# Optimization experiments

Measured on AMD Instinct MI355X. Metric: run time of the kernel, lower is better.

Reference implementation:

```python
import jax, jax.numpy as jnp
import numpy as np

B, N, DM = 4, 4096, 768
H, LH = 12, 4          # total heads, local heads
GH = H - LH            # global (FAVOR+) heads
DH = DM // H           # 64, head dim
M = 256                # nb random features
W = 128                # local window size
EPS = 1e-4


def _gaussian_orthogonal_matrix(m, d, rng):
    # performer-pytorch gaussian_orthogonal_random_matrix, scaling=0
    blocks = []
    for _ in range(int(np.ceil(m / d))):
        q, _ = np.linalg.qr(rng.standard_normal((d, d)))
        blocks.append(q.T)
    mat = np.concatenate(blocks, 0)[:m]
    multiplier = np.linalg.norm(rng.standard_normal((m, d)), axis=-1)
    return (multiplier[:, None] * mat).astype(np.float32)


def setup_inputs() -> dict:
    key = jax.random.key(0)
    ks = jax.random.split(key, 6)
    s = 0.02
    x = jax.random.normal(ks[0], (B, N, DM), jnp.float32)
    mask = jnp.ones((B, N), dtype=bool)
    Wq = jax.random.normal(ks[1], (DM, DM), jnp.float32) * s
    Wk = jax.random.normal(ks[2], (DM, DM), jnp.float32) * s
    Wv = jax.random.normal(ks[3], (DM, DM), jnp.float32) * s
    Wo = jax.random.normal(ks[4], (DM, DM), jnp.float32) * s
    bo = jnp.zeros((DM,), jnp.float32)
    proj = jnp.asarray(_gaussian_orthogonal_matrix(M, DH, np.random.default_rng(0)))
    return {"x": x, "mask": mask, "Wq": Wq, "Wk": Wk, "Wv": Wv,
            "Wo": Wo, "bo": bo, "proj": proj}


def _softmax_kernel(data, proj, is_query):
    # FAVOR+ positive random features for the softmax kernel
    d = data.shape[-1]
    normalizer = d ** -0.25
    ratio = proj.shape[0] ** -0.5
    dd = jnp.einsum('bhnd,md->bhnm', data * normalizer, proj)
    diag = jnp.sum(data ** 2, axis=-1) * 0.5 * (normalizer ** 2)  # (b,h,n)
    if is_query:
        stab = jnp.max(dd, axis=-1, keepdims=True)
        return ratio * (jnp.exp(dd - diag[..., None] - stab) + EPS)
    stab = jnp.max(dd)
    return ratio * (jnp.exp(dd - diag[..., None] - stab) + EPS)


def _favor_attention(q, k, v, proj):
    # non-causal linear attention: O(n * m * d)
    qp = _softmax_kernel(q, proj, True)    # (b,gh,n,m)
    kp = _softmax_kernel(k, proj, False)   # (b,gh,n,m)
    k_sum = kp.sum(axis=2)                               # (b,gh,m)
    d_inv = 1.0 / jnp.einsum('bhnm,bhm->bhn', qp, k_sum)
    context = jnp.einsum('bhnm,bhnd->bhmd', kp, v)       # (b,gh,m,d)
    return jnp.einsum('bhmd,bhnm,bhn->bhnd', context, qp, d_inv)


def _rotary(x):
    # SinusoidalEmbeddings + apply_rotary_pos_emb (NeoX half-rotation)
    n, d = x.shape[-2], x.shape[-1]
    half = d // 2
    inv_freq = 1.0 / (10000.0 ** (jnp.arange(0, d, 2, dtype=jnp.float32) / d))
    freqs = jnp.arange(n, dtype=jnp.float32)[:, None] * inv_freq[None, :]
    emb = jnp.concatenate([freqs, freqs], axis=-1)       # (n,d)
    cos, sin = jnp.cos(emb), jnp.sin(emb)
    x1, x2 = x[..., :half], x[..., half:]
    rot = jnp.concatenate([-x2, x1], axis=-1)
    return x * cos + rot * sin


def _local_attention(lq, lk, lv, mask):
    # windowed attention, look_backward=1, look_forward=1 (non-causal)
    b, h, n, d = lq.shape
    lq, lk = _rotary(lq), _rotary(lk)
    nw = n // W
    bq = lq.reshape(b, h, nw, W, d)
    bk = lk.reshape(b, h, nw, W, d)
    bv = lv.reshape(b, h, nw, W, d)

    def look5(t):  # gather previous/current/next window along window axis
        p = jnp.pad(t, ((0, 0), (0, 0), (1, 1), (0, 0), (0, 0)))
        return jnp.concatenate([p[:, :, i:i + nw] for i in range(3)], axis=3)

    bk, bv = look5(bk), look5(bv)                        # (b,h,nw,3W,d)
    dots = jnp.einsum('bhwie,bhwje->bhwij', bq, bk) * (d ** -0.5)

    ticker = jnp.arange(n).reshape(nw, W)
    tp = jnp.pad(ticker, ((1, 1), (0, 0)), constant_values=-1)
    bq_k = jnp.concatenate([tp[i:i + nw] for i in range(3)], axis=1)  # (nw,3W)
    pad_ok = (bq_k != -1)[None, None, :, None, :]

    mq = mask.reshape(b, nw, W)
    mkp = jnp.pad(mq, ((0, 0), (1, 1), (0, 0)), constant_values=False)
    mk = jnp.concatenate([mkp[:, i:i + nw] for i in range(3)], axis=2)  # (b,nw,3W)
    inp_ok = (mq[:, :, :, None] & mk[:, :, None, :])[:, None]          # (b,1,nw,W,3W)

    neg = -jnp.finfo(dots.dtype).max
    dots = jnp.where(pad_ok & inp_ok, dots, neg)
    attn = jax.nn.softmax(dots, axis=-1)
    out = jnp.einsum('bhwij,bhwje->bhwie', attn, bv)
    return out.reshape(b, h, n, d)


def reference(x, mask, Wq, Wk, Wv, Wo, bo, proj):
    b, n, _ = x.shape
    split = lambda t: t.reshape(b, n, H, DH).transpose(0, 2, 1, 3)  # (b,h,n,d)
    q, k, v = split(x @ Wq), split(x @ Wk), split(x @ Wv)
    qg, lq = q[:, :GH], q[:, GH:]
    kg, lk = k[:, :GH], k[:, GH:]
    vg, lv = v[:, :GH], v[:, GH:]
    # global heads: zero masked values, FAVOR+ linear attention
    vg = jnp.where(mask[:, None, :, None], vg, 0.0)
    out_g = _favor_attention(qg, kg, vg, proj)
    out_l = _local_attention(lq, lk, lv, mask)
    out = jnp.concatenate([out_g, out_l], axis=1)        # (b,H,n,d)
    out = out.transpose(0, 2, 1, 3).reshape(b, n, DM)
    return out @ Wo + bo
```

## Files before the change

### kernel.cpp

```cpp
#include <hip/hip_runtime.h>
#include <hip/hip_fp16.h>
#include <math.h>

#define BB 4
#define NN 4096
#define DMM 768
#define HHH 12
#define LHH 4
#define GHH 8
#define DH 64
#define MM 256
#define WW 128
#define NWIN (NN/WW)
#define EPSF 1.0e-4f
#define NRM 0.35355339059327373f
#define NRM2 0.125f
#define RATIO 0.0625f
#define LN1E4_32 0.28782313662425572f
#define KSTAB_BLOCKS (BB * GHH * (NN / 64))

using fp16x8 = __attribute__((ext_vector_type(8))) _Float16;
using f32x4  = __attribute__((ext_vector_type(4))) float;

static __device__ __forceinline__ unsigned short f2h(float x) {
  return __half_as_ushort(__float2half(x));
}
static __device__ __forceinline__ void gload16(const unsigned short* g, unsigned short* l) {
  __builtin_amdgcn_global_load_lds(
      (const __attribute__((address_space(1))) void*)g,
      (__attribute__((address_space(3))) void*)l, 16, 0, 0);
}

__global__ __launch_bounds__(256) void w_split(
    const float* __restrict__ W, unsigned short* __restrict__ Whi)
{
  int o = blockIdx.x * 256 + threadIdx.x;
  int k = o / DMM, n = o % DMM;
  Whi[(size_t)n * DMM + k] = f2h(W[o]);
}

__global__ __launch_bounds__(256) void a_split(
    const float* __restrict__ A, unsigned short* __restrict__ Ahi,
    unsigned short* __restrict__ Alo)
{
  size_t o = ((size_t)blockIdx.x * 256 + threadIdx.x) * 4;
  float4 v = *(const float4*)(A + o);
  float f[4] = {v.x, v.y, v.z, v.w};
  unsigned short hi[4], lo[4];
#pragma unroll
  for (int i = 0; i < 4; ++i) {
    __half h = __float2half(f[i]);
    hi[i] = __half_as_ushort(h);
    lo[i] = f2h(f[i] - __half2float(h));
  }
  *(uint2*)(Ahi + o) = *(uint2*)&hi[0];
  *(uint2*)(Alo + o) = *(uint2*)&lo[0];
}

__global__ __launch_bounds__(256) void gemm_mfma(
    const float* __restrict__ A, const unsigned short* __restrict__ Bhi,
    const float* __restrict__ bias, float* __restrict__ C, int K, int Nc)
{
  __shared__ unsigned short Ah[128][40];
  __shared__ unsigned short Al[128][40];
  __shared__ unsigned short Bh[128][40];

  const int tid = threadIdx.x;
  const int wid = tid >> 6, lane = tid & 63;
  const int quad = lane >> 4, l16 = lane & 15;
  const int row0 = blockIdx.y * 128;
  const int col0 = blockIdx.x * 128;
  const int wm = (wid & 1) * 64, wn = (wid >> 1) * 64;
  const int sr = tid >> 1;
  const int sk = (tid & 1) * 16;

  f32x4 acc[4][4];
  const f32x4 zf = {0.f, 0.f, 0.f, 0.f};
#pragma unroll
  for (int i = 0; i < 4; ++i)
#pragma unroll
    for (int j = 0; j < 4; ++j) acc[i][j] = zf;

  for (int k0 = 0; k0 < K; k0 += 32) {
    __syncthreads();
    {
      const float* a = A + (size_t)(row0 + sr) * K + k0 + sk;
      float fv[16];
      *(float4*)&fv[0]  = *(const float4*)(a);
      *(float4*)&fv[4]  = *(const float4*)(a + 4);
      *(float4*)&fv[8]  = *(const float4*)(a + 8);
      *(float4*)&fv[12] = *(const float4*)(a + 12);
      unsigned hw[8], lw[8];
#pragma unroll
      for (int p = 0; p < 8; ++p) {
        float x0 = fv[2 * p], x1 = fv[2 * p + 1];
        __half h0 = __float2half(x0), h1 = __float2half(x1);
        unsigned short l0 = f2h(x0 - __half2float(h0));
        unsigned short l1 = f2h(x1 - __half2float(h1));
        hw[p] = (unsigned)__half_as_ushort(h0) | ((unsigned)__half_as_ushort(h1) << 16);
        lw[p] = (unsigned)l0 | ((unsigned)l1 << 16);
      }
      *(uint4*)&Ah[sr][sk]     = *(uint4*)&hw[0];
      *(uint4*)&Ah[sr][sk + 8] = *(uint4*)&hw[4];
      *(uint4*)&Al[sr][sk]     = *(uint4*)&lw[0];
      *(uint4*)&Al[sr][sk + 8] = *(uint4*)&lw[4];
    }
    {
      const unsigned short* bh = Bhi + (size_t)(col0 + sr) * DMM + k0 + sk;
      *(uint4*)&Bh[sr][sk]     = *(const uint4*)(bh);
      *(uint4*)&Bh[sr][sk + 8] = *(const uint4*)(bh + 8);
    }
    __syncthreads();

    fp16x8 afh[4], afl[4], bfh[4];
#pragma unroll
    for (int t = 0; t < 4; ++t) {
      afh[t] = *(const fp16x8*)&Ah[wm + t * 16 + l16][quad * 8];
      afl[t] = *(const fp16x8*)&Al[wm + t * 16 + l16][quad * 8];
      bfh[t] = *(const fp16x8*)&Bh[wn + t * 16 + l16][quad * 8];
    }
#pragma unroll
    for (int ti = 0; ti < 4; ++ti)
#pragma unroll
      for (int tj = 0; tj < 4; ++tj) {
        acc[ti][tj] = __builtin_amdgcn_mfma_f32_16x16x32_f16(afh[ti], bfh[tj], acc[ti][tj], 0, 0, 0);
        acc[ti][tj] = __builtin_amdgcn_mfma_f32_16x16x32_f16(afl[ti], bfh[tj], acc[ti][tj], 0, 0, 0);
      }
  }

  float bv[4] = {0.f, 0.f, 0.f, 0.f};
  if (bias) {
#pragma unroll
    for (int tj = 0; tj < 4; ++tj) bv[tj] = bias[col0 + wn + tj * 16 + l16];
  }
#pragma unroll
  for (int ti = 0; ti < 4; ++ti) {
    const int gr = row0 + wm + ti * 16 + quad * 4;
#pragma unroll
    for (int tj = 0; tj < 4; ++tj) {
      const int gc = col0 + wn + tj * 16 + l16;
      float* cp = C + (size_t)gr * Nc + gc;
#pragma unroll
      for (int r = 0; r < 4; ++r)
        cp[(size_t)r * Nc] = acc[ti][tj][r] + bv[tj];
    }
  }
}

__global__ __launch_bounds__(256) void gemm_mfma_pre(
    const unsigned short* __restrict__ Ahi, const unsigned short* __restrict__ Alo,
    const unsigned short* __restrict__ Bhi,
    const float* __restrict__ bias, float* __restrict__ C, int K, int Nc)
{
  __shared__ unsigned short Ah[128][32];
  __shared__ unsigned short Al[128][32];
  __shared__ unsigned short Bh[128][32];

  const int tid = threadIdx.x;
  const int wid = tid >> 6, lane = tid & 63;
  const int quad = lane >> 4, l16 = lane & 15;

  const int nwg = gridDim.x * gridDim.y;
  int hw = blockIdx.y * gridDim.x + blockIdx.x;
  int logical = ((nwg & 7) == 0) ? ((hw & 7) * (nwg >> 3) + (hw >> 3)) : hw;
  const int col0 = (logical % gridDim.x) * 128;
  const int row0 = (logical / gridDim.x) * 128;

  const int wm = (wid & 1) * 64, wn = (wid >> 1) * 64;
  const int sw8 = (quad ^ ((l16 >> 1) & 3)) * 8;
// ... 42 lines not shown
        acc[ti][tj] = __builtin_amdgcn_mfma_f32_16x16x32_f16(afl[ti], bfh[tj], acc[ti][tj], 0, 0, 0);
      }
  }

  float bv[4] = {0.f, 0.f, 0.f, 0.f};
  if (bias) {
#pragma unroll
    for (int tj = 0; tj < 4; ++tj) bv[tj] = bias[col0 + wn + tj * 16 + l16];
  }
#pragma unroll
  for (int ti = 0; ti < 4; ++ti) {
    const int gr = row0 + wm + ti * 16 + quad * 4;
#pragma unroll
    for (int tj = 0; tj < 4; ++tj) {
      const int gc = col0 + wn + tj * 16 + l16;
      float* cp = C + (size_t)gr * Nc + gc;
#pragma unroll
      for (int r = 0; r < 4; ++r)
        cp[(size_t)r * Nc] = acc[ti][tj][r] + bv[tj];
    }
  }
}

__global__ __launch_bounds__(256) void transpose_proj(
    const float* __restrict__ proj,
    unsigned short* __restrict__ phh, unsigned short* __restrict__ phl)
{
  int o = blockIdx.x * 256 + threadIdx.x;
  int k = o >> 8, m = o & 255;
  float v = proj[m * 64 + k];
  __half hh = __float2half(v);
  float lf = v - __half2float(hh);
  phh[m * 64 + k] = __half_as_ushort(hh);
  phl[m * 64 + k] = f2h(lf);
}

__global__ __launch_bounds__(256) void rot_qk(
    const float* __restrict__ Qb, const float* __restrict__ Kb,
    unsigned short* __restrict__ Qlh, unsigned short* __restrict__ Klh)
{
  int idx = blockIdx.x * 256 + threadIdx.x;
  int n = idx & (NN - 1);
  int bh = idx >> 12;
  int b = bh >> 2, h = bh & 3;
  const float* qs = Qb + ((size_t)(b * NN + n)) * DMM + GHH * DH + h * DH;
  const float* ks = Kb + ((size_t)(b * NN + n)) * DMM + GHH * DH + h * DH;
  float q[64], k[64];
#pragma unroll
  for (int t = 0; t < 16; ++t) {
    *(float4*)&q[t * 4] = *(const float4*)(qs + t * 4);
    *(float4*)&k[t * 4] = *(const float4*)(ks + t * 4);
  }
  unsigned short qo[64], ko[64];
#pragma unroll
  for (int i = 0; i < 32; ++i) {
    float invf = __expf((float)i * -LN1E4_32);
    float th = (float)n * invf;
    float s, c;
    sincosf(th, &s, &c);
    qo[i]      = f2h(fmaf(q[i], c, -q[i + 32] * s) * NRM2);
    qo[i + 32] = f2h(fmaf(q[i + 32], c, q[i] * s) * NRM2);
    ko[i]      = f2h(fmaf(k[i], c, -k[i + 32] * s));
    ko[i + 32] = f2h(fmaf(k[i + 32], c, k[i] * s));
  }
  unsigned short* qd = Qlh + (size_t)idx * 64;
  unsigned short* kd = Klh + (size_t)idx * 64;
#pragma unroll
  for (int t = 0; t < 8; ++t) {
    *(uint4*)(qd + t * 8) = *(uint4*)&qo[t * 8];
    *(uint4*)(kd + t * 8) = *(uint4*)&ko[t * 8];
  }
}

__global__ __launch_bounds__(256) void v_trans(
    const float* __restrict__ Vb, unsigned short* __restrict__ Vt)
{
  __shared__ unsigned short T[64][72];
  const int nb = blockIdx.x, h = blockIdx.y, b = blockIdx.z;
  const int n0 = nb * 64;
  const int tid = threadIdx.x;
  {
    int r = tid >> 2, g = tid & 3;
    const float* src = Vb + ((size_t)(b * NN + n0 + r)) * DMM + GHH * DH + h * DH + g * 16;
#pragma unroll
    for (int t = 0; t < 4; ++t) {
      float4 v = *(const float4*)(src + t * 4);
      T[g * 16 + t * 4 + 0][r] = f2h(v.x);
      T[g * 16 + t * 4 + 1][r] = f2h(v.y);
      T[g * 16 + t * 4 + 2][r] = f2h(v.z);
      T[g * 16 + t * 4 + 3][r] = f2h(v.w);
    }
  }
  __syncthreads();
  {
    int d = tid >> 2, g = tid & 3;
    unsigned short* dst = Vt + ((size_t)(b * LHH + h) * DH + d) * NN + n0 + g * 16;
    *(uint4*)dst       = *(uint4*)&T[d][g * 16];
    *(uint4*)(dst + 8) = *(uint4*)&T[d][g * 16 + 8];
  }
}

__global__ __launch_bounds__(256) void local_attn2(
    const unsigned short* __restrict__ Qlh, const unsigned short* __restrict__ Klh,
    const unsigned short* __restrict__ Vt, float* __restrict__ Qb)
{
  __shared__ unsigned short Pl[4][32][72];
  const int w = blockIdx.x, h = blockIdx.y, b = blockIdx.z;
  const int tid = threadIdx.x;
  const int wid = tid >> 6, lane = tid & 63;
  const int quad = lane >> 4, l16 = lane & 15;
  const int bh = b * LHH + h;
  const int qn0 = w * WW + wid * 32;

  fp16x8 Aq[2][2];
#pragma unroll
  for (int mt = 0; mt < 2; ++mt)
#pragma unroll
    for (int ks = 0; ks < 2; ++ks)
      Aq[mt][ks] = *(const fp16x8*)(Qlh + ((size_t)bh * NN + qn0 + mt * 16 + l16) * 64 + ks * 32 + quad * 8);

  float m_run[8], l_run[8];
  f32x4 Oacc[2][4];
  const f32x4 zf = {0.f, 0.f, 0.f, 0.f};
#pragma unroll
  for (int r = 0; r < 8; ++r) { m_run[r] = -3.4e38f; l_run[r] = 0.f; }
#pragma unroll
  for (int mt = 0; mt < 2; ++mt)
// ... 68 lines not shown
        fp16x8 Ap[2];
#pragma unroll
        for (int mt = 0; mt < 2; ++mt)
          Ap[mt] = *(const fp16x8*)&Pl[wid][mt * 16 + l16][kstep * 32 + quad * 8];
        fp16x8 Bv[4];
#pragma unroll
        for (int nt = 0; nt < 4; ++nt)
          Bv[nt] = *(const fp16x8*)(Vt + ((size_t)bh * DH + nt * 16 + l16) * NN + kn0 + kstep * 32 + quad * 8);
#pragma unroll
        for (int mt = 0; mt < 2; ++mt)
#pragma unroll
          for (int nt = 0; nt < 4; ++nt)
            Oacc[mt][nt] = __builtin_amdgcn_mfma_f32_16x16x32_f16(Ap[mt], Bv[nt], Oacc[mt][nt], 0, 0, 0);
      }
    }
  }

#pragma unroll
  for (int mt = 0; mt < 2; ++mt)
#pragma unroll
    for (int reg = 0; reg < 4; ++reg) {
      const float inv = 1.0f / l_run[mt * 4 + reg];
      const int n = qn0 + mt * 16 + quad * 4 + reg;
      float* dst = Qb + ((size_t)(b * NN + n)) * DMM + GHH * DH + h * DH;
#pragma unroll
      for (int nt = 0; nt < 4; ++nt)
        dst[nt * 16 + l16] = Oacc[mt][nt][reg] * inv;
    }
}

__global__ __launch_bounds__(256) void favor_kstab_mfma(
    const float* __restrict__ Kg, const unsigned short* __restrict__ phh,
    const unsigned short* __restrict__ phl, float* __restrict__ stabp)
{
  __shared__ unsigned short Khh[64][72];
  __shared__ unsigned short Khl[64][72];
  __shared__ float wred[4];
  const int tid = threadIdx.x;
  const int wid = tid >> 6, lane = tid & 63;
  const int quad = lane >> 4, l16 = lane & 15;
  const int chunk = blockIdx.x & 63;
  const int bh = blockIdx.x >> 6;
  const int b = bh >> 3, h = bh & 7;
  const int n0 = chunk * 64;
  const f32x4 zf = {0.f, 0.f, 0.f, 0.f};

  {
    const int r = tid >> 2, s2 = tid & 3;
    const float* ksrc = Kg + ((size_t)(b * NN + n0 + r)) * DMM + h * DH + s2 * 16;
    unsigned short th[16], tl[16];
#pragma unroll
    for (int t = 0; t < 4; ++t) {
      float4 g = *(const float4*)(ksrc + t * 4);
      float f[4] = {g.x * NRM, g.y * NRM, g.z * NRM, g.w * NRM};
#pragma unroll
      for (int j = 0; j < 4; ++j) {
        __half hh = __float2half(f[j]);
        th[t * 4 + j] = __half_as_ushort(hh);
        tl[t * 4 + j] = f2h(f[j] - __half2float(hh));
      }
    }
    *(uint4*)&Khh[r][s2 * 16]     = *(uint4*)&th[0];
    *(uint4*)&Khh[r][s2 * 16 + 8] = *(uint4*)&th[8];
    *(uint4*)&Khl[r][s2 * 16]     = *(uint4*)&tl[0];
    *(uint4*)&Khl[r][s2 * 16 + 8] = *(uint4*)&tl[8];
  }
  __syncthreads();

  const int wn0 = wid * 64;
  f32x4 acc[4][4];
#pragma unroll
  for (int i = 0; i < 4; ++i)
#pragma unroll
    for (int j = 0; j < 4; ++j) acc[i][j] = zf;

#pragma unroll
  for (int ks = 0; ks < 2; ++ks) {
    fp16x8 afh[4], afl[4], bfh[4], bfl[4];
#pragma unroll
    for (int t = 0; t < 4; ++t) {
      afh[t] = *(const fp16x8*)&Khh[t * 16 + l16][ks * 32 + quad * 8];
      afl[t] = *(const fp16x8*)&Khl[t * 16 + l16][ks * 32 + quad * 8];
      const size_t po = (size_t)(wn0 + t * 16 + l16) * 64 + ks * 32 + quad * 8;
      bfh[t] = *(const fp16x8*)(phh + po);
      bfl[t] = *(const fp16x8*)(phl + po);
    }
#pragma unroll
    for (int mt = 0; mt < 4; ++mt)
// ... 16 lines not shown
  for (int off = 32; off; off >>= 1) mx = fmaxf(mx, __shfl_xor(mx, off));
  if (lane == 0) wred[wid] = mx;
  __syncthreads();
  if (tid == 0)
    stabp[blockIdx.x] = fmaxf(fmaxf(wred[0], wred[1]), fmaxf(wred[2], wred[3]));
}

__global__ __launch_bounds__(256) void stab_reduce(
    const float* __restrict__ stabp, float* __restrict__ stab_f)
{
  __shared__ float wred[4];
  const int tid = threadIdx.x;
  float m = -3.4e38f;
  for (int i = tid; i < KSTAB_BLOCKS; i += 256) m = fmaxf(m, stabp[i]);
#pragma unroll
  for (int off = 32; off; off >>= 1) m = fmaxf(m, __shfl_xor(m, off));
  if ((tid & 63) == 0) wred[tid >> 6] = m;
  __syncthreads();
  if (tid == 0)
    *stab_f = fmaxf(fmaxf(wred[0], wred[1]), fmaxf(wred[2], wred[3]));
}

__global__ __launch_bounds__(256, 2) void favor_ctx_mfma(
    const float* __restrict__ Kg, const float* __restrict__ Vg,
    const unsigned short* __restrict__ phh, const unsigned short* __restrict__ phl,
    const float* __restrict__ stab_f,
    float* __restrict__ ctxp, float* __restrict__ ksump, int split)
{
  __shared__ unsigned short Khh[64][72];
  __shared__ unsigned short Khl[64][72];
  __shared__ unsigned short Vt_h[64][72];
  __shared__ unsigned short kp_s[256][72];
  __shared__ float diag_s[64];

  const int tid = threadIdx.x;
  const int wid = tid >> 6, lane = tid & 63;
  const int quad = lane >> 4, l16 = lane & 15;
  const int sidx = blockIdx.x % split;
  const int bh = blockIdx.x / split;
  const int b = bh >> 3, h = bh & 7;
  const int rows = NN / split, nch = rows / 64;
  const float stab = *stab_f;
  const int wn0 = wid * 64;
  const f32x4 zf = {0.f, 0.f, 0.f, 0.f};

  f32x4 acc2[4][4];
#pragma unroll
  for (int i = 0; i < 4; ++i)
#pragma unroll
    for (int j = 0; j < 4; ++j) acc2[i][j] = zf;
  float ksacc[4] = {0.f, 0.f, 0.f, 0.f};

  for (int c = 0; c < nch; ++c) {
    const int n0 = sidx * rows + c * 64;
    __syncthreads();
    {
      const int r = tid >> 2, s2 = tid & 3;
      const float* ksrc = Kg + ((size_t)(b * NN + n0 + r)) * DMM + h * DH + s2 * 16;
      const float* vsrc = Vg + ((size_t)(b * NN + n0 + r)) * DMM + h * DH + s2 * 16;
      float kq = 0.f;
      unsigned short th[16], tl[16];
#pragma unroll
      for (int t = 0; t < 4; ++t) {
        float4 g = *(const float4*)(ksrc + t * 4);
        float f[4] = {g.x * NRM, g.y * NRM, g.z * NRM, g.w * NRM};
#pragma unroll
        for (int j = 0; j < 4; ++j) {
          kq = fmaf(f[j], f[j], kq);
          __half hh = __float2half(f[j]);
          th[t * 4 + j] = __half_as_ushort(hh);
          tl[t * 4 + j] = f2h(f[j] - __half2float(hh));
        }
        float4 vv = *(const float4*)(vsrc + t * 4);
        Vt_h[s2 * 16 + t * 4 + 0][r] = f2h(vv.x);
        Vt_h[s2 * 16 + t * 4 + 1][r] = f2h(vv.y);
        Vt_h[s2 * 16 + t * 4 + 2][r] = f2h(vv.z);
        Vt_h[s2 * 16 + t * 4 + 3][r] = f2h(vv.w);
      }
      *(uint4*)&Khh[r][s2 * 16]     = *(uint4*)&th[0];
      *(uint4*)&Khh[r][s2 * 16 + 8] = *(uint4*)&th[8];
      *(uint4*)&Khl[r][s2 * 16]     = *(uint4*)&tl[0];
      *(uint4*)&Khl[r][s2 * 16 + 8] = *(uint4*)&tl[8];
      kq += __shfl_xor(kq, 1);
      kq += __shfl_xor(kq, 2);
      if (s2 == 0) diag_s[r] = 0.5f * kq;
    }
    __syncthreads();

    f32x4 acc[4][4];
#pragma unroll
    for (int i = 0; i < 4; ++i)
#pragma unroll
      for (int j = 0; j < 4; ++j) acc[i][j] = zf;
#pragma unroll
    for (int ks = 0; ks < 2; ++ks) {
      fp16x8 afh[4], afl[4], bfh[4], bfl[4];
#pragma unroll
      for (int t = 0; t < 4; ++t) {
        afh[t] = *(const fp16x8*)&Khh[t * 16 + l16][ks * 32 + quad * 8];
        afl[t] = *(const fp16x8*)&Khl[t * 16 + l16][ks * 32 + quad * 8];
        const size_t po = (size_t)(wn0 + t * 16 + l16) * 64 + ks * 32 + quad * 8;
        bfh[t] = *(const fp16x8*)(phh + po);
        bfl[t] = *(const fp16x8*)(phl + po);
      }
#pragma unroll
      for (int mt = 0; mt < 4; ++mt)
#pragma unroll
        for (int nt = 0; nt < 4; ++nt) {
// ... 68 lines not shown
}

__global__ __launch_bounds__(256) void favor_reduce(
    const float* __restrict__ ctxp, const float* __restrict__ ksump,
    unsigned short* __restrict__ ctxT_h, float* __restrict__ ksum, int split)
{
  int i = blockIdx.x * 256 + threadIdx.x;
  if (i < BB * GHH * MM * DH) {
    int bh = i / (MM * DH);
    int md = i % (MM * DH);
    float s = 0.f;
    for (int k = 0; k < split; ++k) s += ctxp[((size_t)(bh * split + k)) * MM * DH + md];
    ctxT_h[i] = f2h(s);
  }
  if (i < BB * GHH * MM) {
    int bh = i / MM, m = i % MM;
    float s = 0.f;
    for (int k = 0; k < split; ++k) s += ksump[(bh * split + k) * MM + m];
    ksum[i] = s;
  }
}

__global__ __launch_bounds__(256, 4) void favor_out_mfma(
    float* __restrict__ Q, const unsigned short* __restrict__ phh,
    const unsigned short* __restrict__ phl,
    const unsigned short* __restrict__ ctxT_h, const float* __restrict__ ksum)
{
  __shared__ union {
    struct { unsigned short Qhh[64][72]; unsigned short Qhl[64][72]; } a;
    unsigned short qp[64][264];
  } sm;
  __shared__ float red[4][64];
  __shared__ float dred[4][64];
  __shared__ float diag4[64][4];
  __shared__ float diag_s[64];
  __shared__ float dinv_s[64];
  __shared__ float ksum_s[256];

  const int tid = threadIdx.x;
  const int wid = tid >> 6, lane = tid & 63;
  const int quad = lane >> 4, l16 = lane & 15;
  const int bh = blockIdx.x >> 6;
  const int chunk = blockIdx.x & 63;
  const int b = bh >> 3, h = bh & 7;
  const int n0 = chunk * 64;
  const f32x4 zf = {0.f, 0.f, 0.f, 0.f};

  {
    const int r = tid >> 2, s2 = tid & 3;
    const float* src = Q + ((size_t)(b * NN + n0 + r)) * DMM + h * DH + s2 * 16;
    float sq = 0.f;
    unsigned short th[16], tl[16];
#pragma unroll
    for (int t = 0; t < 4; ++t) {
      float4 g = *(const float4*)(src + t * 4);
      float f[4] = {g.x * NRM, g.y * NRM, g.z * NRM, g.w * NRM};
#pragma unroll
      for (int j = 0; j < 4; ++j) {
        sq = fmaf(f[j], f[j], sq);
        __half hh = __float2half(f[j]);
        th[t * 4 + j] = __half_as_ushort(hh);
        tl[t * 4 + j] = f2h(f[j] - __half2float(hh));
      }
    }
    diag4[r][s2] = sq;
    *(uint4*)&sm.a.Qhh[r][s2 * 16]     = *(uint4*)&th[0];
    *(uint4*)&sm.a.Qhh[r][s2 * 16 + 8] = *(uint4*)&th[8];
    *(uint4*)&sm.a.Qhl[r][s2 * 16]     = *(uint4*)&tl[0];
    *(uint4*)&sm.a.Qhl[r][s2 * 16 + 8] = *(uint4*)&tl[8];
    ksum_s[tid] = ksum[bh * MM + tid];
  }
  __syncthreads();
  if (tid < 64)
    diag_s[tid] = 0.5f * (diag4[tid][0] + diag4[tid][1] + diag4[tid][2] + diag4[tid][3]);

  const int wn0 = wid * 64;
  f32x4 acc[4][4];
#pragma unroll
  for (int i = 0; i < 4; ++i)
#pragma unroll
    for (int j = 0; j < 4; ++j) acc[i][j] = zf;

#pragma unroll
  for (int ks = 0; ks < 2; ++ks) {
    fp16x8 afh[4], afl[4], bfh[4], bfl[4];
#pragma unroll
    for (int t = 0; t < 4; ++t) {
      afh[t] = *(const fp16x8*)&sm.a.Qhh[t * 16 + l16][ks * 32 + quad * 8];
      afl[t] = *(const fp16x8*)&sm.a.Qhl[t * 16 + l16][ks * 32 + quad * 8];
      const size_t po = (size_t)(wn0 + t * 16 + l16) * 64 + ks * 32 + quad * 8;
      bfh[t] = *(const fp16x8*)(phh + po);
      bfl[t] = *(const fp16x8*)(phl + po);
    }
#pragma unroll
    for (int mt = 0; mt < 4; ++mt)
#pragma unroll
      for (int nt = 0; nt < 4; ++nt) {
// ... 50 lines not shown

  const int wn2 = wid * 16;
  f32x4 acc2[4];
#pragma unroll
  for (int mt = 0; mt < 4; ++mt) acc2[mt] = zf;
#pragma unroll
  for (int ksp = 0; ksp < 8; ++ksp) {
    fp16x8 bv = *(const fp16x8*)(ctxT_h + ((size_t)bh * DH + wn2 + l16) * MM + ksp * 32 + quad * 8);
    fp16x8 ap[4];
#pragma unroll
    for (int mt = 0; mt < 4; ++mt)
      ap[mt] = *(const fp16x8*)&sm.qp[mt * 16 + l16][ksp * 32 + quad * 8];
#pragma unroll
    for (int mt = 0; mt < 4; ++mt)
      acc2[mt] = __builtin_amdgcn_mfma_f32_16x16x32_f16(ap[mt], bv, acc2[mt], 0, 0, 0);
  }
  __syncthreads();

#pragma unroll
  for (int mt = 0; mt < 4; ++mt)
#pragma unroll
    for (int reg = 0; reg < 4; ++reg) {
      const int row = mt * 16 + quad * 4 + reg;
      Q[((size_t)(b * NN + n0 + row)) * DMM + h * DH + wn2 + l16] =
          acc2[mt][reg] * dinv_s[row];
    }
}

extern "C" void kernel_launch(void* const* d_in, const int* in_sizes, int n_in,
                              void* d_out, int out_size, void* d_ws, size_t ws_size,
                              hipStream_t stream)
{
  (void)in_sizes; (void)n_in; (void)out_size;
  const float* x    = (const float*)d_in[0];
  const float* Wq   = (const float*)d_in[2];
  const float* Wk   = (const float*)d_in[3];
  const float* Wv   = (const float*)d_in[4];
  const float* Wo   = (const float*)d_in[5];
  const float* bo   = (const float*)d_in[6];
  const float* proj = (const float*)d_in[7];
  float* out = (float*)d_out;

  const size_t WSZ = (size_t)DMM * DMM;
  const size_t XSP = (size_t)BB * NN * DMM;
  const size_t wbuf_f = (4 * WSZ * 2 + 3) / 4;
  const size_t LSZ = (size_t)BB * LHH * NN * DH;
  const size_t lbuf_f = (3 * LSZ * 2 + 3) / 4;
  const size_t fixed_f = (size_t)3 * XSP + (size_t)BB * GHH * MM * DH
                       + (size_t)BB * GHH * MM + KSTAB_BLOCKS + 16 + MM * DH + 16
                       + wbuf_f + 16 + lbuf_f + 16;

  int split = 8, use_pre = 0;
  for (int s = 32; s >= 8; s >>= 1) {
    size_t part = (size_t)BB * GHH * s * (MM * DH + MM);
    size_t region = part > XSP ? part : XSP;
    if ((fixed_f + region) * 4 <= ws_size) { split = s; use_pre = 1; break; }
  }
  if (!use_pre) {
    for (int s = 32; s >= 8; s >>= 1) {
      size_t need = (fixed_f + (size_t)BB * GHH * s * (MM * DH + MM)) * 4;
      if (need <= ws_size) { split = s; break; }
    }
  }
  size_t part_f = (size_t)BB * GHH * split * (MM * DH + MM);
  size_t region_f = (use_pre && XSP > part_f) ? XSP : part_f;

  float* Qb    = (float*)d_ws;
  float* Kb    = Qb + XSP;
  float* Vb    = Kb + XSP;
  float* region = Vb + XSP;
  float* ctxp  = region;
  float* ksump = ctxp + (size_t)BB * GHH * split * MM * DH;
  unsigned short* xH = (unsigned short*)region;
  unsigned short* xL = xH + XSP;
  float* ctx   = region + region_f;
  unsigned short* ctxT_h = (unsigned short*)ctx;
  float* ksum  = ctx + (size_t)BB * GHH * MM * DH;
  float* stabp = ksum + BB * GHH * MM;
  float* stab_f = stabp + KSTAB_BLOCKS;
  unsigned short* proj_hh = (unsigned short*)(stab_f + 16);
  unsigned short* proj_hl = proj_hh + MM * DH;
  unsigned short* wsp = proj_hl + MM * DH;
  unsigned short* WqH = wsp;
  unsigned short* WkH = wsp + WSZ;
  unsigned short* WvH = wsp + 2 * WSZ;
  unsigned short* WoH = wsp + 3 * WSZ;
  unsigned short* Qlh = wsp + 4 * WSZ;
  unsigned short* Klh = Qlh + LSZ;
  unsigned short* Vtl = Klh + LSZ;

  dim3 blk(256);
  dim3 mg(DMM / 128, (BB * NN) / 128);
  const int wgrid = (int)(WSZ / 256);
  const int agrid = (int)(XSP / 1024);

  w_split<<<wgrid, blk, 0, stream>>>(Wq, WqH);
  w_split<<<wgrid, blk, 0, stream>>>(Wk, WkH);
  w_split<<<wgrid, blk, 0, stream>>>(Wv, WvH);
  w_split<<<wgrid, blk, 0, stream>>>(Wo, WoH);
  if (use_pre) {
    a_split<<<agrid, blk, 0, stream>>>(x, xH, xL);
    gemm_mfma_pre<<<mg, blk, 0, stream>>>(xH, xL, WqH, nullptr, Qb, DMM, DMM);
    gemm_mfma_pre<<<mg, blk, 0, stream>>>(xH, xL, WkH, nullptr, Kb, DMM, DMM);
    gemm_mfma_pre<<<mg, blk, 0, stream>>>(xH, xL, WvH, nullptr, Vb, DMM, DMM);
  } else {
    gemm_mfma<<<mg, blk, 0, stream>>>(x, WqH, nullptr, Qb, DMM, DMM);
    gemm_mfma<<<mg, blk, 0, stream>>>(x, WkH, nullptr, Kb, DMM, DMM);
    gemm_mfma<<<mg, blk, 0, stream>>>(x, WvH, nullptr, Vb, DMM, DMM);
  }
  rot_qk<<<(BB * LHH * NN) / 256, blk, 0, stream>>>(Qb, Kb, Qlh, Klh);
  v_trans<<<dim3(NN / 64, LHH, BB), blk, 0, stream>>>(Vb, Vtl);
  transpose_proj<<<64, blk, 0, stream>>>(proj, proj_hh, proj_hl);
  favor_kstab_mfma<<<KSTAB_BLOCKS, blk, 0, stream>>>(Kb, proj_hh, proj_hl, stabp);
  stab_reduce<<<1, blk, 0, stream>>>(stabp, stab_f);
  favor_ctx_mfma<<<BB * GHH * split, blk, 0, stream>>>(Kb, Vb, proj_hh, proj_hl, stab_f, ctxp, ksump, split);
  favor_reduce<<<(BB * GHH * MM * DH) / 256, blk, 0, stream>>>(ctxp, ksump, ctxT_h, ksum, split);
  favor_out_mfma<<<BB * GHH * (NN / 64), blk, 0, stream>>>(Qb, proj_hh, proj_hl, ctxT_h, ksum);
  local_attn2<<<dim3(NWIN, LHH, BB), blk, 0, stream>>>(Qlh, Klh, Vtl, Qb);
  if (use_pre) {
    a_split<<<agrid, blk, 0, stream>>>(Qb, xH, xL);
    gemm_mfma_pre<<<mg, blk, 0, stream>>>(xH, xL, WoH, bo, out, DMM, DMM);
  } else {
    gemm_mfma<<<mg, blk, 0, stream>>>(Qb, WoH, bo, out, DMM, DMM);
  }
}
```

Before: 534.8 us.

## Store Q/K/V projections as fp16 hi/lo pairs and fuse attention-output splitting

The QKV GEMMs now write fp16 hi/lo split outputs directly, V as hi only, instead of fp32. All downstream kernels read these half-precision buffers, so the per-kernel fp32-to-fp16 split work and fp32 traffic go away. The NRM scaling is folded into the projection matrix, with the diag terms rescaled by NRM2 to match. The favor and local attention kernels write their outputs as split hi/lo directly, which removes the separate a_split pass before the output GEMM. The fallback non-pre GEMM path is deleted, and V rounded to a single fp16 slightly changes numerics in the global heads.

```diff
diff --git a/kernel.cpp b/kernel.cpp
--- a/kernel.cpp
+++ b/kernel.cpp
@@ -25,6 +25,10 @@
 static __device__ __forceinline__ unsigned short f2h(float x) {
   return __half_as_ushort(__float2half(x));
 }
+static __device__ __forceinline__ float h2f(unsigned short u) {
+  union { unsigned short s; _Float16 f; } cv; cv.s = u;
+  return (float)cv.f;
+}
 static __device__ __forceinline__ void gload16(const unsigned short* g, unsigned short* l) {
   __builtin_amdgcn_global_load_lds(
       (const __attribute__((address_space(1))) void*)g,
@@ -49,102 +53,11 @@
   unsigned short hi[4], lo[4];
 #pragma unroll
   for (int i = 0; i < 4; ++i) {
-    __half h = __float2half(f[i]);
-    hi[i] = __half_as_ushort(h);
-    lo[i] = f2h(f[i] - __half2float(h));
+    hi[i] = f2h(f[i]);
+    lo[i] = f2h(f[i] - h2f(hi[i]));
   }
   *(uint2*)(Ahi + o) = *(uint2*)&hi[0];
   *(uint2*)(Alo + o) = *(uint2*)&lo[0];
-}
-
-__global__ __launch_bounds__(256) void gemm_mfma(
-    const float* __restrict__ A, const unsigned short* __restrict__ Bhi,
-    const float* __restrict__ bias, float* __restrict__ C, int K, int Nc)
-{
-  __shared__ unsigned short Ah[128][40];
-  __shared__ unsigned short Al[128][40];
-  __shared__ unsigned short Bh[128][40];
-
-  const int tid = threadIdx.x;
-  const int wid = tid >> 6, lane = tid & 63;
-  const int quad = lane >> 4, l16 = lane & 15;
-  const int row0 = blockIdx.y * 128;
-  const int col0 = blockIdx.x * 128;
-  const int wm = (wid & 1) * 64, wn = (wid >> 1) * 64;
-  const int sr = tid >> 1;
-  const int sk = (tid & 1) * 16;
-
-  f32x4 acc[4][4];
-  const f32x4 zf = {0.f, 0.f, 0.f, 0.f};
-#pragma unroll
-  for (int i = 0; i < 4; ++i)
-#pragma unroll
-    for (int j = 0; j < 4; ++j) acc[i][j] = zf;
-
-  for (int k0 = 0; k0 < K; k0 += 32) {
-    __syncthreads();
-    {
-      const float* a = A + (size_t)(row0 + sr) * K + k0 + sk;
-      float fv[16];
-      *(float4*)&fv[0]  = *(const float4*)(a);
-      *(float4*)&fv[4]  = *(const float4*)(a + 4);
-      *(float4*)&fv[8]  = *(const float4*)(a + 8);
-      *(float4*)&fv[12] = *(const float4*)(a + 12);
-      unsigned hw[8], lw[8];
-#pragma unroll
-      for (int p = 0; p < 8; ++p) {
-        float x0 = fv[2 * p], x1 = fv[2 * p + 1];
-        __half h0 = __float2half(x0), h1 = __float2half(x1);
-        unsigned short l0 = f2h(x0 - __half2float(h0));
-        unsigned short l1 = f2h(x1 - __half2float(h1));
-        hw[p] = (unsigned)__half_as_ushort(h0) | ((unsigned)__half_as_ushort(h1) << 16);
-        lw[p] = (unsigned)l0 | ((unsigned)l1 << 16);
-      }
-      *(uint4*)&Ah[sr][sk]     = *(uint4*)&hw[0];
-      *(uint4*)&Ah[sr][sk + 8] = *(uint4*)&hw[4];
-      *(uint4*)&Al[sr][sk]     = *(uint4*)&lw[0];
-      *(uint4*)&Al[sr][sk + 8] = *(uint4*)&lw[4];
-    }
-    {
-      const unsigned short* bh = Bhi + (size_t)(col0 + sr) * DMM + k0 + sk;
-      *(uint4*)&Bh[sr][sk]     = *(const uint4*)(bh);
-      *(uint4*)&Bh[sr][sk + 8] = *(const uint4*)(bh + 8);
-    }
-    __syncthreads();
-
-    fp16x8 afh[4], afl[4], bfh[4];
-#pragma unroll
-    for (int t = 0; t < 4; ++t) {
-      afh[t] = *(const fp16x8*)&Ah[wm + t * 16 + l16][quad * 8];
-      afl[t] = *(const fp16x8*)&Al[wm + t * 16 + l16][quad * 8];
-      bfh[t] = *(const fp16x8*)&Bh[wn + t * 16 + l16][quad * 8];
-    }
-#pragma unroll
-    for (int ti = 0; ti < 4; ++ti)
-#pragma unroll
-      for (int tj = 0; tj < 4; ++tj) {
-        acc[ti][tj] = __builtin_amdgcn_mfma_f32_16x16x32_f16(afh[ti], bfh[tj], acc[ti][tj], 0, 0, 0);
-        acc[ti][tj] = __builtin_amdgcn_mfma_f32_16x16x32_f16(afl[ti], bfh[tj], acc[ti][tj], 0, 0, 0);
-      }
-  }
-
-  float bv[4] = {0.f, 0.f, 0.f, 0.f};
-  if (bias) {
-#pragma unroll
-    for (int tj = 0; tj < 4; ++tj) bv[tj] = bias[col0 + wn + tj * 16 + l16];
-  }
-#pragma unroll
-  for (int ti = 0; ti < 4; ++ti) {
-    const int gr = row0 + wm + ti * 16 + quad * 4;
-#pragma unroll
-    for (int tj = 0; tj < 4; ++tj) {
-      const int gc = col0 + wn + tj * 16 + l16;
-      float* cp = C + (size_t)gr * Nc + gc;
-#pragma unroll
-      for (int r = 0; r < 4; ++r)
-        cp[(size_t)r * Nc] = acc[ti][tj][r] + bv[tj];
-    }
-  }
 }
 
 __global__ __launch_bounds__(256) void gemm_mfma_pre(
@@ -233,34 +146,118 @@
   }
 }
 
+__global__ __launch_bounds__(256) void gemm_mfma_sp(
+    const unsigned short* __restrict__ Ahi, const unsigned short* __restrict__ Alo,
+    const unsigned short* __restrict__ Bhi,
+    unsigned short* __restrict__ Chi, unsigned short* __restrict__ Clo,
+    int K, int Nc)
+{
+  __shared__ unsigned short Ah[128][32];
+  __shared__ unsigned short Al[128][32];
+  __shared__ unsigned short Bh[128][32];
+
+  const int tid = threadIdx.x;
+  const int wid = tid >> 6, lane = tid & 63;
+  const int quad = lane >> 4, l16 = lane & 15;
+
+  const int nwg = gridDim.x * gridDim.y;
+  int hw = blockIdx.y * gridDim.x + blockIdx.x;
+  int logical = ((nwg & 7) == 0) ? ((hw & 7) * (nwg >> 3) + (hw >> 3)) : hw;
+  const int col0 = (logical % gridDim.x) * 128;
+  const int row0 = (logical / gridDim.x) * 128;
+
+  const int wm = (wid & 1) * 64, wn = (wid >> 1) * 64;
+  const int sw8 = (quad ^ ((l16 >> 1) & 3)) * 8;
+
+  const int rr = tid >> 2;
+  const int cg8 = ((tid & 3) ^ ((tid >> 3) & 3)) * 8;
+
+  f32x4 acc[4][4];
+  const f32x4 zf = {0.f, 0.f, 0.f, 0.f};
+#pragma unroll
+  for (int i = 0; i < 4; ++i)
+#pragma unroll
+    for (int j = 0; j < 4; ++j) acc[i][j] = zf;
+
+  for (int k0 = 0; k0 < K; k0 += 32) {
+    __syncthreads();
+    {
+      const size_t ro0 = (size_t)(row0 + rr) * K + k0 + cg8;
+      const size_t ro1 = (size_t)(row0 + 64 + rr) * K + k0 + cg8;
+      const size_t co0 = (size_t)(col0 + rr) * K + k0 + cg8;
+      const size_t co1 = (size_t)(col0 + 64 + rr) * K + k0 + cg8;
+      unsigned short* la  = &Ah[0][0] + tid * 8;
+      unsigned short* lal = &Al[0][0] + tid * 8;
+      unsigned short* lb  = &Bh[0][0] + tid * 8;
+      gload16(Ahi + ro0, la);
+      gload16(Ahi + ro1, la + 2048);
+      gload16(Alo + ro0, lal);
+      gload16(Alo + ro1, lal + 2048);
+      gload16(Bhi + co0, lb);
+      gload16(Bhi + co1, lb + 2048);
+    }
+    __syncthreads();
+
+    fp16x8 afh[4], afl[4], bfh[4];
+#pragma unroll
+    for (int t = 0; t < 4; ++t) {
+      afh[t] = *(const fp16x8*)&Ah[wm + t * 16 + l16][sw8];
+      afl[t] = *(const fp16x8*)&Al[wm + t * 16 + l16][sw8];
+      bfh[t] = *(const fp16x8*)&Bh[wn + t * 16 + l16][sw8];
+    }
+#pragma unroll
+    for (int ti = 0; ti < 4; ++ti)
+#pragma unroll
+      for (int tj = 0; tj < 4; ++tj) {
+        acc[ti][tj] = __builtin_amdgcn_mfma_f32_16x16x32_f16(afh[ti], bfh[tj], acc[ti][tj], 0, 0, 0);
+        acc[ti][tj] = __builtin_amdgcn_mfma_f32_16x16x32_f16(afl[ti], bfh[tj], acc[ti][tj], 0, 0, 0);
+      }
+  }
+
+#pragma unroll
+  for (int ti = 0; ti < 4; ++ti) {
+    const int gr = row0 + wm + ti * 16 + quad * 4;
+#pragma unroll
+    for (int tj = 0; tj < 4; ++tj) {
+      const int gc = col0 + wn + tj * 16 + l16;
+#pragma unroll
+      for (int r = 0; r < 4; ++r) {
+        float c = acc[ti][tj][r];
+        unsigned short hi = f2h(c);
+        Chi[(size_t)(gr + r) * Nc + gc] = hi;
+        if (Clo) Clo[(size_t)(gr + r) * Nc + gc] = f2h(c - h2f(hi));
+      }
+    }
+  }
+}
+
 __global__ __launch_bounds__(256) void transpose_proj(
     const float* __restrict__ proj,
     unsigned short* __restrict__ phh, unsigned short* __restrict__ phl)
 {
   int o = blockIdx.x * 256 + threadIdx.x;
   int k = o >> 8, m = o & 255;
-  float v = proj[m * 64 + k];
-  __half hh = __float2half(v);
-  float lf = v - __half2float(hh);
-  phh[m * 64 + k] = __half_as_ushort(hh);
-  phl[m * 64 + k] = f2h(lf);
+  float v = proj[m * 64 + k] * NRM;
+  unsigned short hh = f2h(v);
+  phh[m * 64 + k] = hh;
+  phl[m * 64 + k] = f2h(v - h2f(hh));
 }
 
 __global__ __launch_bounds__(256) void rot_qk(
-    const float* __restrict__ Qb, const float* __restrict__ Kb,
+    const unsigned short* __restrict__ QhH, const unsigned short* __restrict__ KhH,
     unsigned short* __restrict__ Qlh, unsigned short* __restrict__ Klh)
 {
   int idx = blockIdx.x * 256 + threadIdx.x;
   int n = idx & (NN - 1);
   int bh = idx >> 12;
   int b = bh >> 2, h = bh & 3;
-  const float* qs = Qb + ((size_t)(b * NN + n)) * DMM + GHH * DH + h * DH;
-  const float* ks = Kb + ((size_t)(b * NN + n)) * DMM + GHH * DH + h * DH;
-  float q[64], k[64];
-#pragma unroll
-  for (int t = 0; t < 16; ++t) {
-    *(float4*)&q[t * 4] = *(const float4*)(qs + t * 4);
-    *(float4*)&k[t * 4] = *(const float4*)(ks + t * 4);
+  const unsigned short* qs = QhH + ((size_t)(b * NN + n)) * DMM + GHH * DH + h * DH;
+  const unsigned short* ks = KhH + ((size_t)(b * NN + n)) * DMM + GHH * DH + h * DH;
+  unsigned short qr[64], kr[64];
+#pragma unroll
+  for (int t = 0; t < 8; ++t) {
+    *(uint4*)&qr[t * 8] = *(const uint4*)(qs + t * 8);
+    *(uint4*)&kr[t * 8] = *(const uint4*)(ks + t * 8);
   }
   unsigned short qo[64], ko[64];
 #pragma unroll
@@ -269,10 +266,12 @@
     float th = (float)n * invf;
     float s, c;
     sincosf(th, &s, &c);
-    qo[i]      = f2h(fmaf(q[i], c, -q[i + 32] * s) * NRM2);
-    qo[i + 32] = f2h(fmaf(q[i + 32], c, q[i] * s) * NRM2);
-    ko[i]      = f2h(fmaf(k[i], c, -k[i + 32] * s));
-    ko[i + 32] = f2h(fmaf(k[i + 32], c, k[i] * s));
+    float q1 = h2f(qr[i]), q2 = h2f(qr[i + 32]);
+    float k1 = h2f(kr[i]), k2 = h2f(kr[i + 32]);
+    qo[i]      = f2h(fmaf(q1, c, -q2 * s) * NRM2);
+    qo[i + 32] = f2h(fmaf(q2, c, q1 * s) * NRM2);
+    ko[i]      = f2h(fmaf(k1, c, -k2 * s));
+    ko[i + 32] = f2h(fmaf(k2, c, k1 * s));
   }
   unsigned short* qd = Qlh + (size_t)idx * 64;
   unsigned short* kd = Klh + (size_t)idx * 64;
@@ -284,7 +283,7 @@
 }
 
 __global__ __launch_bounds__(256) void v_trans(
-    const float* __restrict__ Vb, unsigned short* __restrict__ Vt)
+    const unsigned short* __restrict__ VhH, unsigned short* __restrict__ Vt)
 {
   __shared__ unsigned short T[64][72];
   const int nb = blockIdx.x, h = blockIdx.y, b = blockIdx.z;
@@ -292,15 +291,12 @@
   const int tid = threadIdx.x;
   {
     int r = tid >> 2, g = tid & 3;
-    const float* src = Vb + ((size_t)(b * NN + n0 + r)) * DMM + GHH * DH + h * DH + g * 16;
-#pragma unroll
-    for (int t = 0; t < 4; ++t) {
-      float4 v = *(const float4*)(src + t * 4);
-      T[g * 16 + t * 4 + 0][r] = f2h(v.x);
-      T[g * 16 + t * 4 + 1][r] = f2h(v.y);
-      T[g * 16 + t * 4 + 2][r] = f2h(v.z);
-      T[g * 16 + t * 4 + 3][r] = f2h(v.w);
-    }
+    const unsigned short* src = VhH + ((size_t)(b * NN + n0 + r)) * DMM + GHH * DH + h * DH + g * 16;
+    unsigned short v[16];
+    *(uint4*)&v[0] = *(const uint4*)src;
+    *(uint4*)&v[8] = *(const uint4*)(src + 8);
+#pragma unroll
+    for (int j = 0; j < 16; ++j) T[g * 16 + j][r] = v[j];
   }
   __syncthreads();
   {
@@ -313,7 +309,8 @@
 
 __global__ __launch_bounds__(256) void local_attn2(
     const unsigned short* __restrict__ Qlh, const unsigned short* __restrict__ Klh,
-    const unsigned short* __restrict__ Vt, float* __restrict__ Qb)
+    const unsigned short* __restrict__ Vt,
+    unsigned short* __restrict__ xH, unsigned short* __restrict__ xL)
 {
   __shared__ unsigned short Pl[4][32][72];
   const int w = blockIdx.x, h = blockIdx.y, b = blockIdx.z;
@@ -428,16 +425,21 @@
     for (int reg = 0; reg < 4; ++reg) {
       const float inv = 1.0f / l_run[mt * 4 + reg];
       const int n = qn0 + mt * 16 + quad * 4 + reg;
-      float* dst = Qb + ((size_t)(b * NN + n)) * DMM + GHH * DH + h * DH;
-#pragma unroll
-      for (int nt = 0; nt < 4; ++nt)
-        dst[nt * 16 + l16] = Oacc[mt][nt][reg] * inv;
+      const size_t base = ((size_t)(b * NN + n)) * DMM + GHH * DH + h * DH;
+#pragma unroll
+      for (int nt = 0; nt < 4; ++nt) {
+        float o = Oacc[mt][nt][reg] * inv;
+        unsigned short hi = f2h(o);
+        xH[base + nt * 16 + l16] = hi;
+        xL[base + nt * 16 + l16] = f2h(o - h2f(hi));
+      }
     }
 }
 
 __global__ __launch_bounds__(256) void favor_kstab_mfma(
-    const float* __restrict__ Kg, const unsigned short* __restrict__ phh,
-    const unsigned short* __restrict__ phl, float* __restrict__ stabp)
+    const unsigned short* __restrict__ KhH, const unsigned short* __restrict__ KhL,
+    const unsigned short* __restrict__ phh, const unsigned short* __restrict__ phl,
+    float* __restrict__ stabp)
 {
   __shared__ unsigned short Khh[64][72];
   __shared__ unsigned short Khl[64][72];
@@ -453,23 +455,11 @@
 
   {
     const int r = tid >> 2, s2 = tid & 3;
-    const float* ksrc = Kg + ((size_t)(b * NN + n0 + r)) * DMM + h * DH + s2 * 16;
-    unsigned short th[16], tl[16];
-#pragma unroll
-    for (int t = 0; t < 4; ++t) {
-      float4 g = *(const float4*)(ksrc + t * 4);
-      float f[4] = {g.x * NRM, g.y * NRM, g.z * NRM, g.w * NRM};
-#pragma unroll
-      for (int j = 0; j < 4; ++j) {
-        __half hh = __float2half(f[j]);
-        th[t * 4 + j] = __half_as_ushort(hh);
-        tl[t * 4 + j] = f2h(f[j] - __half2float(hh));
-      }
-    }
-    *(uint4*)&Khh[r][s2 * 16]     = *(uint4*)&th[0];
-    *(uint4*)&Khh[r][s2 * 16 + 8] = *(uint4*)&th[8];
-    *(uint4*)&Khl[r][s2 * 16]     = *(uint4*)&tl[0];
-    *(uint4*)&Khl[r][s2 * 16 + 8] = *(uint4*)&tl[8];
+    const size_t off = ((size_t)(b * NN + n0 + r)) * DMM + h * DH + s2 * 16;
+    *(uint4*)&Khh[r][s2 * 16]     = *(const uint4*)(KhH + off);
+    *(uint4*)&Khh[r][s2 * 16 + 8] = *(const uint4*)(KhH + off + 8);
+    *(uint4*)&Khl[r][s2 * 16]     = *(const uint4*)(KhL + off);
+    *(uint4*)&Khl[r][s2 * 16 + 8] = *(const uint4*)(KhL + off + 8);
   }
   __syncthreads();
 
@@ -532,7 +522,8 @@
 }
 
 __global__ __launch_bounds__(256, 2) void favor_ctx_mfma(
-    const float* __restrict__ Kg, const float* __restrict__ Vg,
+    const unsigned short* __restrict__ KhH, const unsigned short* __restrict__ KhL,
+    const unsigned short* __restrict__ VhH,
     const unsigned short* __restrict__ phh, const unsigned short* __restrict__ phl,
     const float* __restrict__ stab_f,
     float* __restrict__ ctxp, float* __restrict__ ksump, int split)
@@ -566,34 +557,28 @@
     __syncthreads();
     {
       const int r = tid >> 2, s2 = tid & 3;
-      const float* ksrc = Kg + ((size_t)(b * NN + n0 + r)) * DMM + h * DH + s2 * 16;
-      const float* vsrc = Vg + ((size_t)(b * NN + n0 + r)) * DMM + h * DH + s2 * 16;
+      const size_t off = ((size_t)(b * NN + n0 + r)) * DMM + h * DH + s2 * 16;
+      unsigned short kh[16], kl[16], vv[16];
+      *(uint4*)&kh[0] = *(const uint4*)(KhH + off);
+      *(uint4*)&kh[8] = *(const uint4*)(KhH + off + 8);
+      *(uint4*)&kl[0] = *(const uint4*)(KhL + off);
+      *(uint4*)&kl[8] = *(const uint4*)(KhL + off + 8);
+      *(uint4*)&vv[0] = *(const uint4*)(VhH + off);
+      *(uint4*)&vv[8] = *(const uint4*)(VhH + off + 8);
       float kq = 0.f;
-      unsigned short th[16], tl[16];
-#pragma unroll
-      for (int t = 0; t < 4; ++t) {
-        float4 g = *(const float4*)(ksrc + t * 4);
-        float f[4] = {g.x * NRM, g.y * NRM, g.z * NRM, g.w * NRM};
-#pragma unroll
-        for (int j = 0; j < 4; ++j) {
-          kq = fmaf(f[j], f[j], kq);
-          __half hh = __float2half(f[j]);
-          th[t * 4 + j] = __half_as_ushort(hh);
-          tl[t * 4 + j] = f2h(f[j] - __half2float(hh));
-        }
-        float4 vv = *(const float4*)(vsrc + t * 4);
-        Vt_h[s2 * 16 + t * 4 + 0][r] = f2h(vv.x);
-        Vt_h[s2 * 16 + t * 4 + 1][r] = f2h(vv.y);
-        Vt_h[s2 * 16 + t * 4 + 2][r] = f2h(vv.z);
-        Vt_h[s2 * 16 + t * 4 + 3][r] = f2h(vv.w);
-      }
-      *(uint4*)&Khh[r][s2 * 16]     = *(uint4*)&th[0];
-      *(uint4*)&Khh[r][s2 * 16 + 8] = *(uint4*)&th[8];
-      *(uint4*)&Khl[r][s2 * 16]     = *(uint4*)&tl[0];
-      *(uint4*)&Khl[r][s2 * 16 + 8] = *(uint4*)&tl[8];
+#pragma unroll
+      for (int j = 0; j < 16; ++j) {
+        float f = h2f(kh[j]) + h2f(kl[j]);
+        kq = fmaf(f, f, kq);
+        Vt_h[s2 * 16 + j][r] = vv[j];
+      }
+      *(uint4*)&Khh[r][s2 * 16]     = *(uint4*)&kh[0];
+      *(uint4*)&Khh[r][s2 * 16 + 8] = *(uint4*)&kh[8];
+      *(uint4*)&Khl[r][s2 * 16]     = *(uint4*)&kl[0];
+      *(uint4*)&Khl[r][s2 * 16 + 8] = *(uint4*)&kl[8];
       kq += __shfl_xor(kq, 1);
       kq += __shfl_xor(kq, 2);
-      if (s2 == 0) diag_s[r] = 0.5f * kq;
+      if (s2 == 0) diag_s[r] = 0.5f * NRM2 * kq;
     }
     __syncthreads();
 
@@ -708,9 +693,10 @@
 }
 
 __global__ __launch_bounds__(256, 4) void favor_out_mfma(
-    float* __restrict__ Q, const unsigned short* __restrict__ phh,
-    const unsigned short* __restrict__ phl,
-    const unsigned short* __restrict__ ctxT_h, const float* __restrict__ ksum)
+    const unsigned short* __restrict__ QhH, const unsigned short* __restrict__ QhL,
+    const unsigned short* __restrict__ phh, const unsigned short* __restrict__ phl,
+    const unsigned short* __restrict__ ctxT_h, const float* __restrict__ ksum,
+    unsigned short* __restrict__ xH, unsigned short* __restrict__ xL)
 {
   __shared__ union {
     struct { unsigned short Qhh[64][72]; unsigned short Qhl[64][72]; } a;
@@ -734,31 +720,28 @@
 
   {
     const int r = tid >> 2, s2 = tid & 3;
-    const float* src = Q + ((size_t)(b * NN + n0 + r)) * DMM + h * DH + s2 * 16;
+    const size_t off = ((size_t)(b * NN + n0 + r)) * DMM + h * DH + s2 * 16;
+    unsigned short qh[16], ql[16];
+    *(uint4*)&qh[0] = *(const uint4*)(QhH + off);
+    *(uint4*)&qh[8] = *(const uint4*)(QhH + off + 8);
+    *(uint4*)&ql[0] = *(const uint4*)(QhL + off);
+    *(uint4*)&ql[8] = *(const uint4*)(QhL + off + 8);
     float sq = 0.f;
-    unsigned short th[16], tl[16];
-#pragma unroll
-    for (int t = 0; t < 4; ++t) {
-      float4 g = *(const float4*)(src + t * 4);
-      float f[4] = {g.x * NRM, g.y * NRM, g.z * NRM, g.w * NRM};
-#pragma unroll
-      for (int j = 0; j < 4; ++j) {
-        sq = fmaf(f[j], f[j], sq);
-        __half hh = __float2half(f[j]);
-        th[t * 4 + j] = __half_as_ushort(hh);
-        tl[t * 4 + j] = f2h(f[j] - __half2float(hh));
-      }
+#pragma unroll
+    for (int j = 0; j < 16; ++j) {
+      float f = h2f(qh[j]) + h2f(ql[j]);
+      sq = fmaf(f, f, sq);
     }
     diag4[r][s2] = sq;
-    *(uint4*)&sm.a.Qhh[r][s2 * 16]     = *(uint4*)&th[0];
-    *(uint4*)&sm.a.Qhh[r][s2 * 16 + 8] = *(uint4*)&th[8];
-    *(uint4*)&sm.a.Qhl[r][s2 * 16]     = *(uint4*)&tl[0];
-    *(uint4*)&sm.a.Qhl[r][s2 * 16 + 8] = *(uint4*)&tl[8];
+    *(uint4*)&sm.a.Qhh[r][s2 * 16]     = *(uint4*)&qh[0];
+    *(uint4*)&sm.a.Qhh[r][s2 * 16 + 8] = *(uint4*)&qh[8];
+    *(uint4*)&sm.a.Qhl[r][s2 * 16]     = *(uint4*)&ql[0];
+    *(uint4*)&sm.a.Qhl[r][s2 * 16 + 8] = *(uint4*)&ql[8];
     ksum_s[tid] = ksum[bh * MM + tid];
   }
   __syncthreads();
   if (tid < 64)
-    diag_s[tid] = 0.5f * (diag4[tid][0] + diag4[tid][1] + diag4[tid][2] + diag4[tid][3]);
+    diag_s[tid] = 0.5f * NRM2 * (diag4[tid][0] + diag4[tid][1] + diag4[tid][2] + diag4[tid][3]);
 
   const int wn0 = wid * 64;
   f32x4 acc[4][4];
@@ -855,8 +838,11 @@
 #pragma unroll
     for (int reg = 0; reg < 4; ++reg) {
       const int row = mt * 16 + quad * 4 + reg;
-      Q[((size_t)(b * NN + n0 + row)) * DMM + h * DH + wn2 + l16] =
-          acc2[mt][reg] * dinv_s[row];
+      float o = acc2[mt][reg] * dinv_s[row];
+      const size_t base = ((size_t)(b * NN + n0 + row)) * DMM + h * DH + wn2 + l16;
+      unsigned short hi = f2h(o);
+      xH[base] = hi;
+      xL[base] = f2h(o - h2f(hi));
     }
 }
 
@@ -883,25 +869,21 @@
                        + (size_t)BB * GHH * MM + KSTAB_BLOCKS + 16 + MM * DH + 16
                        + wbuf_f + 16 + lbuf_f + 16;
 
-  int split = 8, use_pre = 0;
+  int split = 8;
   for (int s = 32; s >= 8; s >>= 1) {
     size_t part = (size_t)BB * GHH * s * (MM * DH + MM);
     size_t region = part > XSP ? part : XSP;
-    if ((fixed_f + region) * 4 <= ws_size) { split = s; use_pre = 1; break; }
-  }
-  if (!use_pre) {
-    for (int s = 32; s >= 8; s >>= 1) {
-      size_t need = (fixed_f + (size_t)BB * GHH * s * (MM * DH + MM)) * 4;
-      if (need <= ws_size) { split = s; break; }
-    }
+    if ((fixed_f + region) * 4 <= ws_size) { split = s; break; }
   }
   size_t part_f = (size_t)BB * GHH * split * (MM * DH + MM);
-  size_t region_f = (use_pre && XSP > part_f) ? XSP : part_f;
-
-  float* Qb    = (float*)d_ws;
-  float* Kb    = Qb + XSP;
-  float* Vb    = Kb + XSP;
-  float* region = Vb + XSP;
+  size_t region_f = XSP > part_f ? XSP : part_f;
+
+  unsigned short* QhH = (unsigned short*)d_ws;
+  unsigned short* QhL = QhH + XSP;
+  unsigned short* KhH = QhH + 2 * XSP;
+  unsigned short* KhL = QhH + 3 * XSP;
+  unsigned short* VhH = QhH + 4 * XSP;
+  float* region = (float*)d_ws + 3 * XSP;
   float* ctxp  = region;
   float* ksump = ctxp + (size_t)BB * GHH * split * MM * DH;
   unsigned short* xH = (unsigned short*)region;
@@ -931,29 +913,18 @@
   w_split<<<wgrid, blk, 0, stream>>>(Wk, WkH);
   w_split<<<wgrid, blk, 0, stream>>>(Wv, WvH);
   w_split<<<wgrid, blk, 0, stream>>>(Wo, WoH);
-  if (use_pre) {
-    a_split<<<agrid, blk, 0, stream>>>(x, xH, xL);
-    gemm_mfma_pre<<<mg, blk, 0, stream>>>(xH, xL, WqH, nullptr, Qb, DMM, DMM);
-    gemm_mfma_pre<<<mg, blk, 0, stream>>>(xH, xL, WkH, nullptr, Kb, DMM, DMM);
-    gemm_mfma_pre<<<mg, blk, 0, stream>>>(xH, xL, WvH, nullptr, Vb, DMM, DMM);
-  } else {
-    gemm_mfma<<<mg, blk, 0, stream>>>(x, WqH, nullptr, Qb, DMM, DMM);
-    gemm_mfma<<<mg, blk, 0, stream>>>(x, WkH, nullptr, Kb, DMM, DMM);
-    gemm_mfma<<<mg, blk, 0, stream>>>(x, WvH, nullptr, Vb, DMM, DMM);
-  }
-  rot_qk<<<(BB * LHH * NN) / 256, blk, 0, stream>>>(Qb, Kb, Qlh, Klh);
-  v_trans<<<dim3(NN / 64, LHH, BB), blk, 0, stream>>>(Vb, Vtl);
+  a_split<<<agrid, blk, 0, stream>>>(x, xH, xL);
+  gemm_mfma_sp<<<mg, blk, 0, stream>>>(xH, xL, WqH, QhH, QhL, DMM, DMM);
+  gemm_mfma_sp<<<mg, blk, 0, stream>>>(xH, xL, WkH, KhH, KhL, DMM, DMM);
+  gemm_mfma_sp<<<mg, blk, 0, stream>>>(xH, xL, WvH, VhH, (unsigned short*)0, DMM, DMM);
+  rot_qk<<<(BB * LHH * NN) / 256, blk, 0, stream>>>(QhH, KhH, Qlh, Klh);
+  v_trans<<<dim3(NN / 64, LHH, BB), blk, 0, stream>>>(VhH, Vtl);
   transpose_proj<<<64, blk, 0, stream>>>(proj, proj_hh, proj_hl);
-  favor_kstab_mfma<<<KSTAB_BLOCKS, blk, 0, stream>>>(Kb, proj_hh, proj_hl, stabp);
+  favor_kstab_mfma<<<KSTAB_BLOCKS, blk, 0, stream>>>(KhH, KhL, proj_hh, proj_hl, stabp);
   stab_reduce<<<1, blk, 0, stream>>>(stabp, stab_f);
-  favor_ctx_mfma<<<BB * GHH * split, blk, 0, stream>>>(Kb, Vb, proj_hh, proj_hl, stab_f, ctxp, ksump, split);
+  favor_ctx_mfma<<<BB * GHH * split, blk, 0, stream>>>(KhH, KhL, VhH, proj_hh, proj_hl, stab_f, ctxp, ksump, split);
   favor_reduce<<<(BB * GHH * MM * DH) / 256, blk, 0, stream>>>(ctxp, ksump, ctxT_h, ksum, split);
-  favor_out_mfma<<<BB * GHH * (NN / 64), blk, 0, stream>>>(Qb, proj_hh, proj_hl, ctxT_h, ksum);
-  local_attn2<<<dim3(NWIN, LHH, BB), blk, 0, stream>>>(Qlh, Klh, Vtl, Qb);
-  if (use_pre) {
-    a_split<<<agrid, blk, 0, stream>>>(Qb, xH, xL);
-    gemm_mfma_pre<<<mg, blk, 0, stream>>>(xH, xL, WoH, bo, out, DMM, DMM);
-  } else {
-    gemm_mfma<<<mg, blk, 0, stream>>>(Qb, WoH, bo, out, DMM, DMM);
-  }
-}
+  favor_out_mfma<<<BB * GHH * (NN / 64), blk, 0, stream>>>(QhH, QhL, proj_hh, proj_hl, ctxT_h, ksum, xH, xL);
+  local_attn2<<<dim3(NWIN, LHH, BB), blk, 0, stream>>>(Qlh, Klh, Vtl, xH, xL);
+  gemm_mfma_pre<<<mg, blk, 0, stream>>>(xH, xL, WoH, bo, out, DMM, DMM);
+}
```

Measured after the change: 523.3 us. 1.02x faster.
